# Kernel tuning notes

Measured on AMD Instinct MI355X. Metric: run time of the kernel, lower is better.

## Reference

```python
import jax, jax.numpy as jnp
import numpy as np

U, I, D, E, L = 100000, 50000, 64, 600000, 3
N = U + I  # total nodes in bipartite graph


def setup_inputs() -> dict:
    key = jax.random.key(0)
    k1, k2, k3, k4 = jax.random.split(key, 4)
    user_emb = jax.random.normal(k1, (U, D), dtype=jnp.float32) * 0.1
    item_emb = jax.random.normal(k2, (I, D), dtype=jnp.float32) * 0.1
    # random user-item interactions; symmetrize to build the (U+I)x(U+I) adjacency
    u = jax.random.randint(k3, (E,), 0, U)
    i = jax.random.randint(k4, (E,), 0, I) + U
    edge_src = jnp.concatenate([u, i])  # [2E]
    edge_dst = jnp.concatenate([i, u])  # [2E]
    # symmetric normalization: A_hat[s,d] = 1/sqrt(deg_s * deg_d)
    deg = jax.ops.segment_sum(jnp.ones((2 * E,), jnp.float32), edge_dst, num_segments=N)
    dinv = jnp.where(deg > 0, 1.0 / jnp.sqrt(deg), 0.0)
    edge_vals = dinv[edge_src] * dinv[edge_dst]
    return {
        "user_emb": user_emb,
        "item_emb": item_emb,
        "edge_src": edge_src,
        "edge_dst": edge_dst,
        "edge_vals": edge_vals,
    }


def reference(user_emb, item_emb, edge_src, edge_dst, edge_vals):
    # LightGCN propagation: ego_{k+1} = A_hat @ ego_k, then mean over the L layer outputs
    ego = jnp.concatenate([user_emb, item_emb], axis=0)  # [N, D]
    acc = jnp.zeros_like(ego)
    for _ in range(L):  # fixed small layer count
        msgs = edge_vals[:, None] * ego[edge_src]  # [2E, D] gather + scale
        ego = jax.ops.segment_sum(msgs, edge_dst, num_segments=N)  # SpMM via scatter-add
        acc = acc + ego
    mean_emb = acc / L
    return mean_emb[:U], mean_emb[U:]
```

## Files before the change

kernel.cpp:

```cpp
#include <hip/hip_runtime.h>

#define U_CNT 100000
#define I_CNT 50000
#define D_DIM 64
#define N_NODES 150000
#define CHUNK 2048
#define NBKT 586
#define SCAN_BLK 512
#define CCAP 3584
#define NPG 4

__device__ __forceinline__ float blo(unsigned u) { return __uint_as_float(u << 16); }
__device__ __forceinline__ float bhi(unsigned u) { return __uint_as_float(u & 0xFFFF0000u); }
__device__ __forceinline__ unsigned f2b(float f) {
    unsigned b = __float_as_uint(f);
    return (b + 0x7FFFu + ((b >> 16) & 1u)) >> 16;
}
__device__ __forceinline__ unsigned pack2(float a, float b) {
    return f2b(a) | (f2b(b) << 16);
}

__global__ void bucket_hist(const int* __restrict__ dst, int* __restrict__ H,
                            int NB_B, int nE,
                            const float4* __restrict__ user4,
                            const float4* __restrict__ item4,
                            uint2* __restrict__ ego0, int n4u, int n4) {
    __shared__ int h[NBKT];
    for (int i = threadIdx.x; i < NBKT; i += blockDim.x) h[i] = 0;
    __syncthreads();
    int b = blockIdx.x;
    int beg = b * CHUNK, end = min(nE, beg + CHUNK);
    for (int e = beg + (int)threadIdx.x; e < end; e += blockDim.x)
        atomicAdd(&h[dst[e] >> 8], 1);
    __syncthreads();
    for (int i = threadIdx.x; i < NBKT; i += blockDim.x) H[i * NB_B + b] = h[i];
    int gsz = gridDim.x * blockDim.x;
    for (int i = blockIdx.x * blockDim.x + threadIdx.x; i < n4; i += gsz) {
        float4 f = (i < n4u) ? user4[i] : item4[i - n4u];
        ego0[i] = make_uint2(pack2(f.x, f.y), pack2(f.z, f.w));
    }
}

__global__ void block_sums(const int* __restrict__ in, int* __restrict__ blksum, int n) {
    __shared__ int sm[SCAN_BLK];
    int i = blockIdx.x * SCAN_BLK + threadIdx.x;
    sm[threadIdx.x] = (i < n) ? in[i] : 0;
    __syncthreads();
    for (int off = SCAN_BLK / 2; off > 0; off >>= 1) {
        if (threadIdx.x < off) sm[threadIdx.x] += sm[threadIdx.x + off];
        __syncthreads();
    }
    if (threadIdx.x == 0) blksum[blockIdx.x] = sm[0];
}

__global__ void scan_blksums(const int* __restrict__ blksum, int* __restrict__ blkoff, int nb) {
    __shared__ int sm[1024];
    int t = threadIdx.x;
    int v = (t < nb) ? blksum[t] : 0;
    sm[t] = v;
    __syncthreads();
    for (int off = 1; off < 1024; off <<= 1) {
        int x = (t >= off) ? sm[t - off] : 0;
        __syncthreads();
        sm[t] += x;
        __syncthreads();
    }
    if (t < nb) blkoff[t] = sm[t] - v;
}

__global__ void scan_within(int* __restrict__ H, const int* __restrict__ blkoff, int n) {
    __shared__ int sm[SCAN_BLK];
    int i = blockIdx.x * SCAN_BLK + threadIdx.x;
    int t = threadIdx.x;
    int d = (i < n) ? H[i] : 0;
    sm[t] = d;
    __syncthreads();
    for (int off = 1; off < SCAN_BLK; off <<= 1) {
        int x = (t >= off) ? sm[t - off] : 0;
        __syncthreads();
        sm[t] += x;
        __syncthreads();
    }
    if (i < n) H[i] = blkoff[blockIdx.x] + sm[t] - d;
}

__global__ void bucket_scatter(const int* __restrict__ src, const int* __restrict__ dst,
                               const float* __restrict__ val, const int* __restrict__ Hs,
                               uint2* __restrict__ tmp, int NB_B, int nE) {
    __shared__ int cur[NBKT];
    int b = blockIdx.x;
    for (int i = threadIdx.x; i < NBKT; i += blockDim.x) cur[i] = Hs[i * NB_B + b];
    __syncthreads();
    int beg = b * CHUNK, end = min(nE, beg + CHUNK);
    for (int e = beg + (int)threadIdx.x; e < end; e += blockDim.x) {
        int d = dst[e];
        int pos = atomicAdd(&cur[d >> 8], 1);
        tmp[pos] = make_uint2((unsigned)src[e] | ((unsigned)(d & 255) << 18),
                              __float_as_uint(val[e]));
    }
}

__global__ void bucket_build(const int* __restrict__ Hs, const uint2* __restrict__ tmp,
                             int2* __restrict__ csr, int* __restrict__ row_ptr,
                             int* __restrict__ perm, int NB_B, int nE) {
    __shared__ int hist[256];
    __shared__ int scanbuf[256];
    __shared__ int cur[256];
    __shared__ int db[256];
    __shared__ int dbs[256];
    __shared__ uint2 cache[CCAP];
    int bkt  = blockIdx.x;
    int base = Hs[(size_t)bkt * NB_B];
    int endp = (bkt + 1 < NBKT) ? Hs[(size_t)(bkt + 1) * NB_B] : nE;
    int size = endp - base;
    int nbins = min(256, N_NODES - bkt * 256);
    int t = threadIdx.x;

    hist[t] = 0;
    db[t] = 0;
    __syncthreads();
    bool cached = (size <= CCAP);
    for (int k = t; k < size; k += blockDim.x) {
        uint2 r = tmp[base + k];
        if (cached) cache[k] = r;
        atomicAdd(&hist[(r.x >> 18) & 255], 1);
    }
    __syncthreads();
    int v = hist[t];
    scanbuf[t] = v;
    __syncthreads();
    for (int off = 1; off < 256; off <<= 1) {
        int x = (t >= off) ? scanbuf[t - off] : 0;
        __syncthreads();
        scanbuf[t] += x;
        __syncthreads();
    }
    int ex = scanbuf[t] - v;
    if (t < nbins) row_ptr[bkt * 256 + t] = base + ex;
    cur[t] = ex;
    __syncthreads();
    if (bkt == NBKT - 1) {
        if (t == 0) row_ptr[N_NODES] = nE;
        if (t < 4)  csr[nE + t] = make_int2(0, 0);
    }

    int bin = 255 - min(v, 255);
    int rank = 0;
    if (t < nbins) rank = atomicAdd(&db[bin], 1);
    __syncthreads();
    int v2 = db[t];
    dbs[t] = v2;
    __syncthreads();
    for (int off = 1; off < 256; off <<= 1) {
        int x = (t >= off) ? dbs[t - off] : 0;
        __syncthreads();
        dbs[t] += x;
        __syncthreads();
    }
    if (t < nbins) {
        int ex2 = dbs[bin] - db[bin];
        perm[bkt * 256 + ex2 + rank] = bkt * 256 + t;
    }

    for (int k = t; k < size; k += blockDim.x) {
        uint2 r = cached ? cache[k] : tmp[base + k];
        int f = (r.x >> 18) & 255;
        int p = atomicAdd(&cur[f], 1);
        csr[base + p] = make_int2((int)(r.x & 0x3FFFFu), (int)r.y);
    }
}

__device__ __forceinline__ void fma8(float (&acc)[8], float v, uint4 g) {
    acc[0] = fmaf(v, blo(g.x), acc[0]); acc[1] = fmaf(v, bhi(g.x), acc[1]);
    acc[2] = fmaf(v, blo(g.y), acc[2]); acc[3] = fmaf(v, bhi(g.y), acc[3]);
    acc[4] = fmaf(v, blo(g.z), acc[4]); acc[5] = fmaf(v, bhi(g.z), acc[5]);
    acc[6] = fmaf(v, blo(g.w), acc[6]); acc[7] = fmaf(v, bhi(g.w), acc[7]);
}

template <int FINAL>
__global__ void lgcn_spmm(const int* __restrict__ row_ptr,
                          const int2* __restrict__ csr,
                          const uint4* __restrict__ ego_in,
                          uint4* __restrict__ ego_out,
                          const uint4* __restrict__ egoA,
                          const uint4* __restrict__ egoB,
                          float4* __restrict__ out,
                          const int* __restrict__ perm) {
    int gid = (blockIdx.x * blockDim.x + threadIdx.x) >> 3;
    int l   = threadIdx.x & 7;
    int nbase = gid * NPG;
    if (nbase >= N_NODES) return;

    int4 p4 = *reinterpret_cast<const int4*>(&perm[nbase]);
    int nodes[NPG] = {p4.x, p4.y, p4.z, p4.w};
    int begs[NPG], ends[NPG];
#pragma unroll
    for (int n = 0; n < NPG; ++n) {
        begs[n] = row_ptr[nodes[n]];
        ends[n] = row_ptr[nodes[n] + 1];
    }
    int2 ce[NPG][4];
#pragma unroll
    for (int n = 0; n < NPG; ++n) {
#pragma unroll
        for (int k = 0; k < 4; ++k) ce[n][k] = csr[begs[n] + k];
    }

#pragma unroll
    for (int n = 0; n < NPG; ++n) {
        int node = nodes[n];
        int beg = begs[n], end = ends[n];

        float a0[8] = {0, 0, 0, 0, 0, 0, 0, 0};
        float a1[8] = {0, 0, 0, 0, 0, 0, 0, 0};

        int2 e0 = ce[n][0], e1 = ce[n][1], e2 = ce[n][2], e3 = ce[n][3];
        int j = beg;
        while (j + 4 <= end) {
            uint4 x0 = ego_in[(size_t)e0.x * 8 + l];
            uint4 x1 = ego_in[(size_t)e1.x * 8 + l];
            uint4 x2 = ego_in[(size_t)e2.x * 8 + l];
            uint4 x3 = ego_in[(size_t)e3.x * 8 + l];
            int2 n0 = csr[j + 4], n1 = csr[j + 5], n2 = csr[j + 6], n3 = csr[j + 7];
            fma8(a0, __int_as_float(e0.y), x0);
            fma8(a1, __int_as_float(e1.y), x1);
            fma8(a0, __int_as_float(e2.y), x2);
            fma8(a1, __int_as_float(e3.y), x3);
            e0 = n0; e1 = n1; e2 = n2; e3 = n3;
            j += 4;
        }
        int rem = end - j;
        if (rem > 0) fma8(a0, __int_as_float(e0.y), ego_in[(size_t)e0.x * 8 + l]);
        if (rem > 1) fma8(a1, __int_as_float(e1.y), ego_in[(size_t)e1.x * 8 + l]);
        if (rem > 2) fma8(a0, __int_as_float(e2.y), ego_in[(size_t)e2.x * 8 + l]);

        float acc[8];
#pragma unroll
        for (int k = 0; k < 8; ++k) acc[k] = a0[k] + a1[k];

        if (!FINAL) {
            uint4 r;
            r.x = pack2(acc[0], acc[1]); r.y = pack2(acc[2], acc[3]);
            r.z = pack2(acc[4], acc[5]); r.w = pack2(acc[6], acc[7]);
            ego_out[(size_t)node * 8 + l] = r;
        } else {
            uint4 a = egoA[(size_t)node * 8 + l];
            uint4 b = egoB[(size_t)node * 8 + l];
            const float s = 1.0f / 3.0f;
            float4 o0, o1;
            o0.x = (blo(a.x) + blo(b.x) + acc[0]) * s;
            o0.y = (bhi(a.x) + bhi(b.x) + acc[1]) * s;
            o0.z = (blo(a.y) + blo(b.y) + acc[2]) * s;
            o0.w = (bhi(a.y) + bhi(b.y) + acc[3]) * s;
            o1.x = (blo(a.z) + blo(b.z) + acc[4]) * s;
            o1.y = (bhi(a.z) + bhi(b.z) + acc[5]) * s;
            o1.z = (blo(a.w) + blo(b.w) + acc[6]) * s;
            o1.w = (bhi(a.w) + bhi(b.w) + acc[7]) * s;
            size_t ob = (size_t)node * 16 + 2 * l;
            out[ob]     = o0;
            out[ob + 1] = o1;
        }
    }
}

static inline size_t align_up(size_t x, size_t a) { return (x + a - 1) & ~(a - 1); }

extern "C" void kernel_launch(void* const* d_in, const int* in_sizes, int n_in,
                              void* d_out, int out_size, void* d_ws, size_t ws_size,
                              hipStream_t stream) {
    const float* user_emb  = (const float*)d_in[0];
    const float* item_emb  = (const float*)d_in[1];
    const int*   edge_src  = (const int*)d_in[2];
    const int*   edge_dst  = (const int*)d_in[3];
    const float* edge_vals = (const float*)d_in[4];
    const int    nE        = in_sizes[2];

    float* out = (float*)d_out;
    const size_t nd = (size_t)N_NODES * D_DIM;

    const int NB_B = (nE + CHUNK - 1) / CHUNK;
    const int nH   = NBKT * NB_B;
    const int NBs  = (nH + SCAN_BLK - 1) / SCAN_BLK;

    size_t off = 0;
    char* base = (char*)d_ws;
    int2*  csr     = (int2*)(base + off);  off = align_up(off + (size_t)(nE + 4) * sizeof(int2), 256);
    int*   row_ptr = (int*)(base + off);   off = align_up(off + (size_t)(N_NODES + 1) * 4, 256);
    uint2* tmp     = (uint2*)(base + off); off = align_up(off + (size_t)nE * sizeof(uint2), 256);
    int*   H       = (int*)(base + off);   off = align_up(off + (size_t)nH * 4, 256);
    int*   blksum  = (int*)(base + off);   off = align_up(off + (size_t)NBs * 4, 256);
    int*   blkoff  = (int*)(base + off);   off = align_up(off + (size_t)NBs * 4, 256);
    uint4* ego0    = (uint4*)(base + off); off = align_up(off + (size_t)N_NODES * 128, 256);
    uint4* ego_a   = (uint4*)(base + off); off = align_up(off + (size_t)N_NODES * 128, 256);
    uint4* ego_b   = (uint4*)(base + off); off = align_up(off + (size_t)N_NODES * 128, 256);
    int*   perm    = (int*)(base + off);   off = align_up(off + (size_t)N_NODES * 4, 256);

    const int block = 256;
    const int n4  = (int)(nd / 4);
    const int n4u = U_CNT * D_DIM / 4;

    bucket_hist<<<NB_B, block, 0, stream>>>(edge_dst, H, NB_B, nE,
        (const float4*)user_emb, (const float4*)item_emb, (uint2*)ego0, n4u, n4);
    block_sums<<<NBs, SCAN_BLK, 0, stream>>>(H, blksum, nH);
    scan_blksums<<<1, 1024, 0, stream>>>(blksum, blkoff, NBs);
    scan_within<<<NBs, SCAN_BLK, 0, stream>>>(H, blkoff, nH);
    bucket_scatter<<<NB_B, block, 0, stream>>>(edge_src, edge_dst, edge_vals, H, tmp, NB_B, nE);
    bucket_build<<<NBKT, block, 0, stream>>>(H, tmp, csr, row_ptr, perm, NB_B, nE);

    const size_t threads = ((size_t)N_NODES / NPG) * 8;
    const int spmm_grid = (int)((threads + block - 1) / block);

    lgcn_spmm<0><<<spmm_grid, block, 0, stream>>>(
        row_ptr, csr, ego0, ego_a, nullptr, nullptr, nullptr, perm);
    lgcn_spmm<0><<<spmm_grid, block, 0, stream>>>(
        row_ptr, csr, ego_a, ego_b, nullptr, nullptr, nullptr, perm);
    lgcn_spmm<1><<<spmm_grid, block, 0, stream>>>(
        row_ptr, csr, ego_b, nullptr, ego_a, ego_b, (float4*)out, perm);
}
```

Baseline: 269.0 us.

## Replace per-chunk bucket histogram scan with global atomic bucket cursors

The full chunk-by-bucket histogram and its three-kernel scan are replaced by global per-bucket counts gathered with atomics, a single 586-entry scan, and per-block cursor reservation via atomicAdd inside the scatter kernel. The edge chunk size is doubled. The SpMM kernel now processes one node per 8-lane group instead of four, giving more parallelism and less register pressure. Edge order within a bucket becomes nondeterministic, which can change floating-point summation order, and the scatter kernel now reads dst twice.

```diff
diff --git a/kernel.cpp b/kernel.cpp
--- a/kernel.cpp
+++ b/kernel.cpp
@@ -4,11 +4,9 @@
 #define I_CNT 50000
 #define D_DIM 64
 #define N_NODES 150000
-#define CHUNK 2048
+#define CHUNK 4096
 #define NBKT 586
-#define SCAN_BLK 512
 #define CCAP 3584
-#define NPG 4
 
 __device__ __forceinline__ float blo(unsigned u) { return __uint_as_float(u << 16); }
 __device__ __forceinline__ float bhi(unsigned u) { return __uint_as_float(u & 0xFFFF0000u); }
@@ -20,8 +18,8 @@
     return f2b(a) | (f2b(b) << 16);
 }
 
-__global__ void bucket_hist(const int* __restrict__ dst, int* __restrict__ H,
-                            int NB_B, int nE,
+__global__ void bucket_hist(const int* __restrict__ dst, int* __restrict__ bCnt,
+                            int nE,
                             const float4* __restrict__ user4,
                             const float4* __restrict__ item4,
                             uint2* __restrict__ ego0, int n4u, int n4) {
@@ -33,7 +31,8 @@
     for (int e = beg + (int)threadIdx.x; e < end; e += blockDim.x)
         atomicAdd(&h[dst[e] >> 8], 1);
     __syncthreads();
-    for (int i = threadIdx.x; i < NBKT; i += blockDim.x) H[i * NB_B + b] = h[i];
+    for (int i = threadIdx.x; i < NBKT; i += blockDim.x)
+        if (h[i] > 0) atomicAdd(&bCnt[i], h[i]);
     int gsz = gridDim.x * blockDim.x;
     for (int i = blockIdx.x * blockDim.x + threadIdx.x; i < n4; i += gsz) {
         float4 f = (i < n4u) ? user4[i] : item4[i - n4u];
@@ -41,22 +40,10 @@
     }
 }
 
-__global__ void block_sums(const int* __restrict__ in, int* __restrict__ blksum, int n) {
-    __shared__ int sm[SCAN_BLK];
-    int i = blockIdx.x * SCAN_BLK + threadIdx.x;
-    sm[threadIdx.x] = (i < n) ? in[i] : 0;
-    __syncthreads();
-    for (int off = SCAN_BLK / 2; off > 0; off >>= 1) {
-        if (threadIdx.x < off) sm[threadIdx.x] += sm[threadIdx.x + off];
-        __syncthreads();
-    }
-    if (threadIdx.x == 0) blksum[blockIdx.x] = sm[0];
-}
-
-__global__ void scan_blksums(const int* __restrict__ blksum, int* __restrict__ blkoff, int nb) {
+__global__ void scan586(const int* __restrict__ bCnt, int* __restrict__ bBase, int nE) {
     __shared__ int sm[1024];
     int t = threadIdx.x;
-    int v = (t < nb) ? blksum[t] : 0;
+    int v = (t < NBKT) ? bCnt[t] : 0;
     sm[t] = v;
     __syncthreads();
     for (int off = 1; off < 1024; off <<= 1) {
@@ -65,33 +52,28 @@
         sm[t] += x;
         __syncthreads();
     }
-    if (t < nb) blkoff[t] = sm[t] - v;
-}
-
-__global__ void scan_within(int* __restrict__ H, const int* __restrict__ blkoff, int n) {
-    __shared__ int sm[SCAN_BLK];
-    int i = blockIdx.x * SCAN_BLK + threadIdx.x;
-    int t = threadIdx.x;
-    int d = (i < n) ? H[i] : 0;
-    sm[t] = d;
-    __syncthreads();
-    for (int off = 1; off < SCAN_BLK; off <<= 1) {
-        int x = (t >= off) ? sm[t - off] : 0;
-        __syncthreads();
-        sm[t] += x;
-        __syncthreads();
-    }
-    if (i < n) H[i] = blkoff[blockIdx.x] + sm[t] - d;
+    if (t < NBKT) bBase[t] = sm[t] - v;
+    if (t == 0) bBase[NBKT] = nE;
 }
 
 __global__ void bucket_scatter(const int* __restrict__ src, const int* __restrict__ dst,
-                               const float* __restrict__ val, const int* __restrict__ Hs,
-                               uint2* __restrict__ tmp, int NB_B, int nE) {
+                               const float* __restrict__ val,
+                               const int* __restrict__ bBase, int* __restrict__ bCursor,
+                               uint2* __restrict__ tmp, int nE) {
+    __shared__ int cnt[NBKT];
     __shared__ int cur[NBKT];
     int b = blockIdx.x;
-    for (int i = threadIdx.x; i < NBKT; i += blockDim.x) cur[i] = Hs[i * NB_B + b];
+    for (int i = threadIdx.x; i < NBKT; i += blockDim.x) cnt[i] = 0;
     __syncthreads();
     int beg = b * CHUNK, end = min(nE, beg + CHUNK);
+    for (int e = beg + (int)threadIdx.x; e < end; e += blockDim.x)
+        atomicAdd(&cnt[dst[e] >> 8], 1);
+    __syncthreads();
+    for (int i = threadIdx.x; i < NBKT; i += blockDim.x) {
+        int c = cnt[i];
+        cur[i] = (c > 0) ? (bBase[i] + atomicAdd(&bCursor[i], c)) : 0;
+    }
+    __syncthreads();
     for (int e = beg + (int)threadIdx.x; e < end; e += blockDim.x) {
         int d = dst[e];
         int pos = atomicAdd(&cur[d >> 8], 1);
@@ -100,9 +82,9 @@
     }
 }
 
-__global__ void bucket_build(const int* __restrict__ Hs, const uint2* __restrict__ tmp,
+__global__ void bucket_build(const int* __restrict__ bBase, const uint2* __restrict__ tmp,
                              int2* __restrict__ csr, int* __restrict__ row_ptr,
-                             int* __restrict__ perm, int NB_B, int nE) {
+                             int* __restrict__ perm, int nE) {
     __shared__ int hist[256];
     __shared__ int scanbuf[256];
     __shared__ int cur[256];
@@ -110,8 +92,8 @@
     __shared__ int dbs[256];
     __shared__ uint2 cache[CCAP];
     int bkt  = blockIdx.x;
-    int base = Hs[(size_t)bkt * NB_B];
-    int endp = (bkt + 1 < NBKT) ? Hs[(size_t)(bkt + 1) * NB_B] : nE;
+    int base = bBase[bkt];
+    int endp = bBase[bkt + 1];
     int size = endp - base;
     int nbins = min(256, N_NODES - bkt * 256);
     int t = threadIdx.x;
@@ -186,80 +168,61 @@
                           const uint4* __restrict__ egoB,
                           float4* __restrict__ out,
                           const int* __restrict__ perm) {
-    int gid = (blockIdx.x * blockDim.x + threadIdx.x) >> 3;
-    int l   = threadIdx.x & 7;
-    int nbase = gid * NPG;
-    if (nbase >= N_NODES) return;
-
-    int4 p4 = *reinterpret_cast<const int4*>(&perm[nbase]);
-    int nodes[NPG] = {p4.x, p4.y, p4.z, p4.w};
-    int begs[NPG], ends[NPG];
+    int widx = (blockIdx.x * blockDim.x + threadIdx.x) >> 3;
+    int l    = threadIdx.x & 7;
+    if (widx >= N_NODES) return;
+    int node = perm[widx];
+    int beg = row_ptr[node];
+    int end = row_ptr[node + 1];
+
+    float a0[8] = {0, 0, 0, 0, 0, 0, 0, 0};
+    float a1[8] = {0, 0, 0, 0, 0, 0, 0, 0};
+
+    int2 e0 = csr[beg], e1 = csr[beg + 1], e2 = csr[beg + 2], e3 = csr[beg + 3];
+    int j = beg;
+    while (j + 4 <= end) {
+        uint4 x0 = ego_in[(size_t)e0.x * 8 + l];
+        uint4 x1 = ego_in[(size_t)e1.x * 8 + l];
+        uint4 x2 = ego_in[(size_t)e2.x * 8 + l];
+        uint4 x3 = ego_in[(size_t)e3.x * 8 + l];
+        int2 n0 = csr[j + 4], n1 = csr[j + 5], n2 = csr[j + 6], n3 = csr[j + 7];
+        fma8(a0, __int_as_float(e0.y), x0);
+        fma8(a1, __int_as_float(e1.y), x1);
+        fma8(a0, __int_as_float(e2.y), x2);
+        fma8(a1, __int_as_float(e3.y), x3);
+        e0 = n0; e1 = n1; e2 = n2; e3 = n3;
+        j += 4;
+    }
+    int rem = end - j;
+    if (rem > 0) fma8(a0, __int_as_float(e0.y), ego_in[(size_t)e0.x * 8 + l]);
+    if (rem > 1) fma8(a1, __int_as_float(e1.y), ego_in[(size_t)e1.x * 8 + l]);
+    if (rem > 2) fma8(a0, __int_as_float(e2.y), ego_in[(size_t)e2.x * 8 + l]);
+
+    float acc[8];
 #pragma unroll
-    for (int n = 0; n < NPG; ++n) {
-        begs[n] = row_ptr[nodes[n]];
-        ends[n] = row_ptr[nodes[n] + 1];
-    }
-    int2 ce[NPG][4];
-#pragma unroll
-    for (int n = 0; n < NPG; ++n) {
-#pragma unroll
-        for (int k = 0; k < 4; ++k) ce[n][k] = csr[begs[n] + k];
-    }
-
-#pragma unroll
-    for (int n = 0; n < NPG; ++n) {
-        int node = nodes[n];
-        int beg = begs[n], end = ends[n];
-
-        float a0[8] = {0, 0, 0, 0, 0, 0, 0, 0};
-        float a1[8] = {0, 0, 0, 0, 0, 0, 0, 0};
-
-        int2 e0 = ce[n][0], e1 = ce[n][1], e2 = ce[n][2], e3 = ce[n][3];
-        int j = beg;
-        while (j + 4 <= end) {
-            uint4 x0 = ego_in[(size_t)e0.x * 8 + l];
-            uint4 x1 = ego_in[(size_t)e1.x * 8 + l];
-            uint4 x2 = ego_in[(size_t)e2.x * 8 + l];
-            uint4 x3 = ego_in[(size_t)e3.x * 8 + l];
-            int2 n0 = csr[j + 4], n1 = csr[j + 5], n2 = csr[j + 6], n3 = csr[j + 7];
-            fma8(a0, __int_as_float(e0.y), x0);
-            fma8(a1, __int_as_float(e1.y), x1);
-            fma8(a0, __int_as_float(e2.y), x2);
-            fma8(a1, __int_as_float(e3.y), x3);
-            e0 = n0; e1 = n1; e2 = n2; e3 = n3;
-            j += 4;
-        }
-        int rem = end - j;
-        if (rem > 0) fma8(a0, __int_as_float(e0.y), ego_in[(size_t)e0.x * 8 + l]);
-        if (rem > 1) fma8(a1, __int_as_float(e1.y), ego_in[(size_t)e1.x * 8 + l]);
-        if (rem > 2) fma8(a0, __int_as_float(e2.y), ego_in[(size_t)e2.x * 8 + l]);
-
-        float acc[8];
-#pragma unroll
-        for (int k = 0; k < 8; ++k) acc[k] = a0[k] + a1[k];
-
-        if (!FINAL) {
-            uint4 r;
-            r.x = pack2(acc[0], acc[1]); r.y = pack2(acc[2], acc[3]);
-            r.z = pack2(acc[4], acc[5]); r.w = pack2(acc[6], acc[7]);
-            ego_out[(size_t)node * 8 + l] = r;
-        } else {
-            uint4 a = egoA[(size_t)node * 8 + l];
-            uint4 b = egoB[(size_t)node * 8 + l];
-            const float s = 1.0f / 3.0f;
-            float4 o0, o1;
-            o0.x = (blo(a.x) + blo(b.x) + acc[0]) * s;
-            o0.y = (bhi(a.x) + bhi(b.x) + acc[1]) * s;
-            o0.z = (blo(a.y) + blo(b.y) + acc[2]) * s;
-            o0.w = (bhi(a.y) + bhi(b.y) + acc[3]) * s;
-            o1.x = (blo(a.z) + blo(b.z) + acc[4]) * s;
-            o1.y = (bhi(a.z) + bhi(b.z) + acc[5]) * s;
-            o1.z = (blo(a.w) + blo(b.w) + acc[6]) * s;
-            o1.w = (bhi(a.w) + bhi(b.w) + acc[7]) * s;
-            size_t ob = (size_t)node * 16 + 2 * l;
-            out[ob]     = o0;
-            out[ob + 1] = o1;
-        }
+    for (int k = 0; k < 8; ++k) acc[k] = a0[k] + a1[k];
+
+    if (!FINAL) {
+        uint4 r;
+        r.x = pack2(acc[0], acc[1]); r.y = pack2(acc[2], acc[3]);
+        r.z = pack2(acc[4], acc[5]); r.w = pack2(acc[6], acc[7]);
+        ego_out[(size_t)node * 8 + l] = r;
+    } else {
+        uint4 a = egoA[(size_t)node * 8 + l];
+        uint4 b = egoB[(size_t)node * 8 + l];
+        const float s = 1.0f / 3.0f;
+        float4 o0, o1;
+        o0.x = (blo(a.x) + blo(b.x) + acc[0]) * s;
+        o0.y = (bhi(a.x) + bhi(b.x) + acc[1]) * s;
+        o0.z = (blo(a.y) + blo(b.y) + acc[2]) * s;
+        o0.w = (bhi(a.y) + bhi(b.y) + acc[3]) * s;
+        o1.x = (blo(a.z) + blo(b.z) + acc[4]) * s;
+        o1.y = (bhi(a.z) + bhi(b.z) + acc[5]) * s;
+        o1.z = (blo(a.w) + blo(b.w) + acc[6]) * s;
+        o1.w = (bhi(a.w) + bhi(b.w) + acc[7]) * s;
+        size_t ob = (size_t)node * 16 + 2 * l;
+        out[ob]     = o0;
+        out[ob + 1] = o1;
     }
 }
 
@@ -279,17 +242,15 @@
     const size_t nd = (size_t)N_NODES * D_DIM;
 
     const int NB_B = (nE + CHUNK - 1) / CHUNK;
-    const int nH   = NBKT * NB_B;
-    const int NBs  = (nH + SCAN_BLK - 1) / SCAN_BLK;
 
     size_t off = 0;
     char* base = (char*)d_ws;
     int2*  csr     = (int2*)(base + off);  off = align_up(off + (size_t)(nE + 4) * sizeof(int2), 256);
     int*   row_ptr = (int*)(base + off);   off = align_up(off + (size_t)(N_NODES + 1) * 4, 256);
     uint2* tmp     = (uint2*)(base + off); off = align_up(off + (size_t)nE * sizeof(uint2), 256);
-    int*   H       = (int*)(base + off);   off = align_up(off + (size_t)nH * 4, 256);
-    int*   blksum  = (int*)(base + off);   off = align_up(off + (size_t)NBs * 4, 256);
-    int*   blkoff  = (int*)(base + off);   off = align_up(off + (size_t)NBs * 4, 256);
+    int*   bCnt    = (int*)(base + off);   off = align_up(off + (size_t)NBKT * 4, 256);
+    int*   bCursor = (int*)(base + off);   off = align_up(off + (size_t)NBKT * 4, 256);
+    int*   bBase   = (int*)(base + off);   off = align_up(off + (size_t)(NBKT + 1) * 4, 256);
     uint4* ego0    = (uint4*)(base + off); off = align_up(off + (size_t)N_NODES * 128, 256);
     uint4* ego_a   = (uint4*)(base + off); off = align_up(off + (size_t)N_NODES * 128, 256);
     uint4* ego_b   = (uint4*)(base + off); off = align_up(off + (size_t)N_NODES * 128, 256);
@@ -299,15 +260,15 @@
     const int n4  = (int)(nd / 4);
     const int n4u = U_CNT * D_DIM / 4;
 
-    bucket_hist<<<NB_B, block, 0, stream>>>(edge_dst, H, NB_B, nE,
+    hipMemsetAsync(bCnt, 0, 2 * align_up((size_t)NBKT * 4, 256), stream);
+    bucket_hist<<<NB_B, block, 0, stream>>>(edge_dst, bCnt, nE,
         (const float4*)user_emb, (const float4*)item_emb, (uint2*)ego0, n4u, n4);
-    block_sums<<<NBs, SCAN_BLK, 0, stream>>>(H, blksum, nH);
-    scan_blksums<<<1, 1024, 0, stream>>>(blksum, blkoff, NBs);
-    scan_within<<<NBs, SCAN_BLK, 0, stream>>>(H, blkoff, nH);
-    bucket_scatter<<<NB_B, block, 0, stream>>>(edge_src, edge_dst, edge_vals, H, tmp, NB_B, nE);
-    bucket_build<<<NBKT, block, 0, stream>>>(H, tmp, csr, row_ptr, perm, NB_B, nE);
-
-    const size_t threads = ((size_t)N_NODES / NPG) * 8;
+    scan586<<<1, 1024, 0, stream>>>(bCnt, bBase, nE);
+    bucket_scatter<<<NB_B, block, 0, stream>>>(edge_src, edge_dst, edge_vals,
+                                               bBase, bCursor, tmp, nE);
+    bucket_build<<<NBKT, block, 0, stream>>>(bBase, tmp, csr, row_ptr, perm, nE);
+
+    const size_t threads = (size_t)N_NODES * 8;
     const int spmm_grid = (int)((threads + block - 1) / block);
 
     lgcn_spmm<0><<<spmm_grid, block, 0, stream>>>(
```

After: 271.9 us. About the same (+1.1%).
